# Kernel optimization log

Measured on AMD Instinct MI355X. Metric: run time of the kernel, lower is better.

The kernel has to match this reference:

```python
import jax, jax.numpy as jnp
import numpy as np

B, S, H = 32, 4096, 1024
EPS = 1e-12

def setup_inputs() -> dict:
    key = jax.random.key(0)
    k1, k2, k3, k4 = jax.random.split(key, 4)
    x = jax.random.normal(k1, (B, S, H), dtype=jnp.float32)
    # mask: random bool; force the first two positions True per row so every
    # row has >=2 masked elements (std with ddof=1 is well-defined)
    mask = jax.random.randint(k2, (B, S), 0, 2).astype(bool)
    mask = mask.at[:, :2].set(True)
    W = jax.random.normal(k3, (H,), dtype=jnp.float32) / np.sqrt(H)
    b = jax.random.normal(k4, (1,), dtype=jnp.float32) * 0.01
    return {"input": x, "mask": mask, "W": W, "b": b}

def reference(input, mask, W, b):
    # linear projection hidden_size -> 1, then squeeze -> [B, S]
    h = jnp.einsum("bsh,h->bs", input, W) + b  # [B, S]
    mf = mask.astype(h.dtype)
    n = mf.sum(axis=-1, keepdims=True)                      # [B, 1]
    mean = (h * mf).sum(axis=-1, keepdims=True) / n         # masked mean
    # torch .std() on the masked slice: unbiased (ddof=1)
    var = (((h - mean) ** 2) * mf).sum(axis=-1, keepdims=True) / (n - 1)
    std = jnp.sqrt(var) + EPS
    z = (h - mean) / std
    zmin = jnp.min(jnp.where(mask, z, jnp.inf), axis=-1, keepdims=True)
    zmax = jnp.max(jnp.where(mask, z, -jnp.inf), axis=-1, keepdims=True)
    rescaled = (z - zmin) / (zmax - zmin)
    return (rescaled * mf)[..., None]  # [B, S, 1]
```

## Files before the change

kernel.cpp:

```cpp
#include <hip/hip_runtime.h>

#define BB 32
#define SS 4096
#define HH 1024
#define BS (BB * SS)
#define WPB 256
#define RPW (SS / WPB)
#define NWAVES (BB * WPB)
#define NBLOCKS (NWAVES / 4)

__device__ __forceinline__ unsigned fkey(float f) {
    unsigned u = __float_as_uint(f);
    return (u & 0x80000000u) ? ~u : (u | 0x80000000u);
}
__device__ __forceinline__ float funkey(unsigned k) {
    unsigned u = (k & 0x80000000u) ? (k ^ 0x80000000u) : ~k;
    return __uint_as_float(u);
}
__device__ __forceinline__ float dot4(float4 a, float4 w) {
    return a.x * w.x + a.y * w.y + a.z * w.z + a.w * w.w;
}

__global__ __launch_bounds__(256) void k_proj(
    const float* __restrict__ x, const int* __restrict__ mask,
    const float* __restrict__ W, const float* __restrict__ bvec,
    float* __restrict__ h, unsigned* __restrict__ mm)
{
    const int lane  = threadIdx.x & 63;
    const int gw    = blockIdx.x * 4 + (threadIdx.x >> 6);
    const int batch = gw >> 8;
    const int r0    = gw & (WPB - 1);

    const float4* Wv = (const float4*)W;
    const float4 w0 = Wv[lane], w1 = Wv[64 + lane],
                 w2 = Wv[128 + lane], w3 = Wv[192 + lane];
    const float bval = bvec[0];

    const size_t rowBase = (size_t)batch * SS;
    unsigned kmin = 0xFFFFFFFFu, kmax = 0u;

    const float4* xr = (const float4*)(x + (rowBase + r0) * HH);
    float4 a0 = xr[lane], a1 = xr[64 + lane], a2 = xr[128 + lane], a3 = xr[192 + lane];

    for (int k = 0; k < RPW; ++k) {
        const int r = r0 + k * WPB;
        float4 b0, b1, b2, b3;
        if (k < RPW - 1) {
            const float4* xn = (const float4*)(x + (rowBase + r + WPB) * HH);
            b0 = xn[lane]; b1 = xn[64 + lane]; b2 = xn[128 + lane]; b3 = xn[192 + lane];
        }
        float acc = dot4(a0, w0) + dot4(a1, w1) + dot4(a2, w2) + dot4(a3, w3);
#pragma unroll
        for (int off = 32; off >= 1; off >>= 1)
            acc += __shfl_xor(acc, off, 64);
        const float hv = acc + bval;
        if (lane == 0) h[rowBase + r] = hv;
        if (mask[rowBase + r] != 0) {
            const unsigned key = fkey(hv);
            kmin = min(kmin, key); kmax = max(kmax, key);
        }
        a0 = b0; a1 = b1; a2 = b2; a3 = b3;
    }
    if (lane == 0) {
        atomicMin(&mm[batch], kmin);
        atomicMax(&mm[BB + batch], kmax);
    }
}

__global__ __launch_bounds__(256) void k_final(
    const float* __restrict__ h, const int* __restrict__ mask,
    const unsigned* __restrict__ mm, float* __restrict__ out)
{
    const int i = blockIdx.x * 256 + threadIdx.x;
    if (i >= BS) return;
    const int batch = i >> 12;
    const float hmin = funkey(mm[batch]);
    const float hmax = funkey(mm[BB + batch]);
    const float inv = 1.0f / (hmax - hmin);
    const float v = (h[i] - hmin) * inv;
    out[i] = (mask[i] != 0) ? v : 0.0f;
}

extern "C" void kernel_launch(void* const* d_in, const int* in_sizes, int n_in,
                              void* d_out, int out_size, void* d_ws, size_t ws_size,
                              hipStream_t stream) {
    const float* x    = (const float*)d_in[0];
    const int*   mask = (const int*)d_in[1];
    const float* W    = (const float*)d_in[2];
    const float* bv   = (const float*)d_in[3];
    float* out = (float*)d_out;

    float*    h  = (float*)d_ws;
    unsigned* mm = (unsigned*)((char*)d_ws + (size_t)BS * 4);

    hipMemsetAsync(mm, 0xFF, BB * sizeof(unsigned), stream);
    hipMemsetAsync(mm + BB, 0x00, BB * sizeof(unsigned), stream);

    k_proj<<<NBLOCKS, 256, 0, stream>>>(x, mask, W, bv, h, mm);
    k_final<<<(BS + 255) / 256, 256, 0, stream>>>(h, mask, mm, out);
}
```

Before: 715.5 us.

## Split projection into one-row-per-wave kernel and separate per-batch min/max reduction

The fused projection kernel, where each wave handled 16 rows with software prefetch and atomics, becomes one wave per row with a single load batch and no loop. Masked min/max moves into a new kernel with one block per batch that reads h and the mask. This removes the atomics and the two memsets. The aim is more memory-level parallelism across a much larger grid, at the cost of an extra launch and a small re-read of h.

Measured after the change: 684.2 us. 4.4% less time.

```diff
diff --git a/kernel.cpp b/kernel.cpp
--- a/kernel.cpp
+++ b/kernel.cpp
@@ -4,10 +4,6 @@
 #define SS 4096
 #define HH 1024
 #define BS (BB * SS)
-#define WPB 256
-#define RPW (SS / WPB)
-#define NWAVES (BB * WPB)
-#define NBLOCKS (NWAVES / 4)
 
 __device__ __forceinline__ unsigned fkey(float f) {
     unsigned u = __float_as_uint(f);
@@ -21,49 +17,56 @@
     return a.x * w.x + a.y * w.y + a.z * w.z + a.w * w.w;
 }
 
-__global__ __launch_bounds__(256) void k_proj(
-    const float* __restrict__ x, const int* __restrict__ mask,
-    const float* __restrict__ W, const float* __restrict__ bvec,
-    float* __restrict__ h, unsigned* __restrict__ mm)
+__global__ __launch_bounds__(256, 8) void k_proj(
+    const float* __restrict__ x, const float* __restrict__ W,
+    const float* __restrict__ bvec, float* __restrict__ h)
 {
-    const int lane  = threadIdx.x & 63;
-    const int gw    = blockIdx.x * 4 + (threadIdx.x >> 6);
-    const int batch = gw >> 8;
-    const int r0    = gw & (WPB - 1);
+    const int lane = threadIdx.x & 63;
+    const int row  = blockIdx.x * 4 + (threadIdx.x >> 6);
+
+    const float4* xr = (const float4*)(x + (size_t)row * HH);
+    const float4 a0 = xr[lane],       a1 = xr[64 + lane],
+                 a2 = xr[128 + lane], a3 = xr[192 + lane];
 
     const float4* Wv = (const float4*)W;
-    const float4 w0 = Wv[lane], w1 = Wv[64 + lane],
+    const float4 w0 = Wv[lane],       w1 = Wv[64 + lane],
                  w2 = Wv[128 + lane], w3 = Wv[192 + lane];
-    const float bval = bvec[0];
 
-    const size_t rowBase = (size_t)batch * SS;
+    float acc = dot4(a0, w0) + dot4(a1, w1) + dot4(a2, w2) + dot4(a3, w3);
+#pragma unroll
+    for (int off = 32; off >= 1; off >>= 1)
+        acc += __shfl_xor(acc, off, 64);
+
+    if (lane == 0) h[row] = acc + bvec[0];
+}
+
+__global__ __launch_bounds__(256) void k_minmax(
+    const float* __restrict__ h, const int* __restrict__ mask,
+    unsigned* __restrict__ mm)
+{
+    const int batch = blockIdx.x;
+    const int t = threadIdx.x;
+    const size_t base = (size_t)batch * SS;
+
     unsigned kmin = 0xFFFFFFFFu, kmax = 0u;
-
-    const float4* xr = (const float4*)(x + (rowBase + r0) * HH);
-    float4 a0 = xr[lane], a1 = xr[64 + lane], a2 = xr[128 + lane], a3 = xr[192 + lane];
-
-    for (int k = 0; k < RPW; ++k) {
-        const int r = r0 + k * WPB;
-        float4 b0, b1, b2, b3;
-        if (k < RPW - 1) {
-            const float4* xn = (const float4*)(x + (rowBase + r + WPB) * HH);
-            b0 = xn[lane]; b1 = xn[64 + lane]; b2 = xn[128 + lane]; b3 = xn[192 + lane];
+    for (int i = t; i < SS; i += 256) {
+        if (mask[base + i] != 0) {
+            const unsigned k = fkey(h[base + i]);
+            kmin = min(kmin, k); kmax = max(kmax, k);
         }
-        float acc = dot4(a0, w0) + dot4(a1, w1) + dot4(a2, w2) + dot4(a3, w3);
+    }
 #pragma unroll
-        for (int off = 32; off >= 1; off >>= 1)
-            acc += __shfl_xor(acc, off, 64);
-        const float hv = acc + bval;
-        if (lane == 0) h[rowBase + r] = hv;
-        if (mask[rowBase + r] != 0) {
-            const unsigned key = fkey(hv);
-            kmin = min(kmin, key); kmax = max(kmax, key);
-        }
-        a0 = b0; a1 = b1; a2 = b2; a3 = b3;
+    for (int off = 32; off >= 1; off >>= 1) {
+        kmin = min(kmin, (unsigned)__shfl_xor((int)kmin, off, 64));
+        kmax = max(kmax, (unsigned)__shfl_xor((int)kmax, off, 64));
     }
-    if (lane == 0) {
-        atomicMin(&mm[batch], kmin);
-        atomicMax(&mm[BB + batch], kmax);
+    __shared__ unsigned smin[4], smax[4];
+    if ((t & 63) == 0) { smin[t >> 6] = kmin; smax[t >> 6] = kmax; }
+    __syncthreads();
+    if (t == 0) {
+        const unsigned m0 = min(min(smin[0], smin[1]), min(smin[2], smin[3]));
+        const unsigned M0 = max(max(smax[0], smax[1]), max(smax[2], smax[3]));
+        mm[batch] = m0; mm[BB + batch] = M0;
     }
 }
 
@@ -93,9 +96,7 @@
     float*    h  = (float*)d_ws;
     unsigned* mm = (unsigned*)((char*)d_ws + (size_t)BS * 4);
 
-    hipMemsetAsync(mm, 0xFF, BB * sizeof(unsigned), stream);
-    hipMemsetAsync(mm + BB, 0x00, BB * sizeof(unsigned), stream);
-
-    k_proj<<<NBLOCKS, 256, 0, stream>>>(x, mask, W, bv, h, mm);
+    k_proj<<<BS / 4, 256, 0, stream>>>(x, W, bv, h);
+    k_minmax<<<BB, 256, 0, stream>>>(h, mask, mm);
     k_final<<<(BS + 255) / 256, 256, 0, stream>>>(h, mask, mm, out);
 }
```
